# Kernel tuning notes

Hardware: AMD Instinct MI355X
Metric: run time of the kernel (lower is better)

The kernel has to match this reference:

```python
import jax, jax.numpy as jnp
import numpy as np

OBS_DIM = 64; ACT_DIM = 18; INTER = 64; COMMAND = 32
UNITS = ACT_DIM + COMMAND + INTER  # 114; neuron order: [motor, command, inter]
Q_HIDDEN = max(32, UNITS)
B, T = 2048, 64
ODE_UNFOLDS = 6
EPS = 1e-8


def _build_wiring(seed=0):
    """NCP sparse wiring: sensory->inter, inter->command, command recurrent, command->motor."""
    rng = np.random.default_rng(seed)
    adj = np.zeros((UNITS, UNITS), np.float32)   # [pre, post]
    sens = np.zeros((OBS_DIM, UNITS), np.float32)
    motor = np.arange(ACT_DIM)
    cmd = np.arange(ACT_DIM, ACT_DIM + COMMAND)
    inter = np.arange(ACT_DIM + COMMAND, UNITS)
    for s in range(OBS_DIM):
        for d in rng.choice(inter, size=8, replace=False):
            sens[s, d] = rng.choice([-1.0, 1.0])
    for i in inter:
        for d in rng.choice(cmd, size=8, replace=False):
            adj[i, d] = rng.choice([-1.0, 1.0])
    for _ in range(32):
        adj[rng.choice(cmd), rng.choice(cmd)] = rng.choice([-1.0, 1.0])
    for m in motor:
        for s in rng.choice(cmd, size=8, replace=False):
            adj[s, m] = rng.choice([-1.0, 1.0])
    return adj, sens


def setup_inputs() -> dict:
    key = jax.random.key(0)
    ks = jax.random.split(key, 16)
    adj, sens = _build_wiring()
    u = lambda k, shape, lo, hi: jax.random.uniform(k, shape, jnp.float32, lo, hi)
    return {
        "obs": jax.random.normal(ks[0], (B, T, OBS_DIM), jnp.float32),
        "hidden": jnp.zeros((B, UNITS), jnp.float32),
        "input_w": jnp.ones((OBS_DIM,), jnp.float32),
        "input_b": jnp.zeros((OBS_DIM,), jnp.float32),
        "sensory_w": u(ks[1], (OBS_DIM, UNITS), 0.001, 1.0),
        "sensory_mu": u(ks[2], (OBS_DIM, UNITS), 0.3, 0.8),
        "sensory_sigma": u(ks[3], (OBS_DIM, UNITS), 3.0, 8.0),
        "sensory_erev": jnp.asarray(sens),
        "sensory_mask": jnp.asarray(np.abs(sens)),
        "w": u(ks[4], (UNITS, UNITS), 0.001, 1.0),
        "mu": u(ks[5], (UNITS, UNITS), 0.3, 0.8),
        "sigma": u(ks[6], (UNITS, UNITS), 3.0, 8.0),
        "erev": jnp.asarray(adj),
        "mask": jnp.asarray(np.abs(adj)),
        "gleak": u(ks[7], (UNITS,), 0.001, 1.0),
        "vleak": u(ks[8], (UNITS,), -0.2, 0.2),
        "cm": u(ks[9], (UNITS,), 0.4, 0.6),
        "q_w1": jax.random.normal(ks[10], (UNITS, Q_HIDDEN), jnp.float32) / np.sqrt(UNITS).astype(np.float32),
        "q_b1": jnp.zeros((Q_HIDDEN,), jnp.float32),
        "q_w2": jax.random.normal(ks[11], (Q_HIDDEN, ACT_DIM), jnp.float32) / np.sqrt(Q_HIDDEN).astype(np.float32),
        "q_b2": jnp.zeros((ACT_DIM,), jnp.float32),
    }


def _ltc_forward(obs, hidden, input_w, input_b, sensory_w, sensory_mu, sensory_sigma,
                 sensory_erev, sensory_mask, w, mu, sigma, erev, mask, gleak, vleak, cm):
    sw = sensory_w * sensory_mask          # sparse sensory synapses (S, U)
    ww = w * mask                          # sparse recurrent synapses (U, U)
    cm_t = cm * ODE_UNFOLDS                # cm / (elapsed_time / ode_unfolds), elapsed_time = 1.0

    @jax.checkpoint
    def step(h, x):
        xi = x * input_w + input_b                                                    # (B, S) affine input map
        s_act = sw * jax.nn.sigmoid((xi[:, :, None] - sensory_mu) * sensory_sigma)    # (B, S, U)
        w_num_s = jnp.sum(s_act * sensory_erev, axis=1)                               # (B, U)
        w_den_s = jnp.sum(s_act, axis=1)                                              # (B, U)

        def unfold(v, _):
            act = ww * jax.nn.sigmoid((v[:, :, None] - mu) * sigma)                   # (B, U, U)
            num = cm_t * v + gleak * vleak + jnp.sum(act * erev, axis=1) + w_num_s
            den = cm_t + gleak + jnp.sum(act, axis=1) + w_den_s
            return num / (den + EPS), None

        v, _ = jax.lax.scan(unfold, h, None, length=ODE_UNFOLDS)
        return v, None

    h, _ = jax.lax.scan(step, hidden, jnp.swapaxes(obs, 0, 1))  # scan over time
    return h


def reference(obs, hidden, input_w, input_b, sensory_w, sensory_mu, sensory_sigma,
              sensory_erev, sensory_mask, w, mu, sigma, erev, mask, gleak, vleak, cm,
              q_w1, q_b1, q_w2, q_b2):
    h = _ltc_forward(obs, hidden, input_w, input_b, sensory_w, sensory_mu, sensory_sigma,
                     sensory_erev, sensory_mask, w, mu, sigma, erev, mask, gleak, vleak, cm)
    q = jax.nn.relu(h @ q_w1 + q_b1) @ q_w2 + q_b2  # Q-head over full hidden state
    return q, h
```

## Files before the change

### kernel.cpp

```cpp
#include <hip/hip_runtime.h>

#define UNITS   114
#define SDIM    64
#define ACT     18
#define TSTEPS  64

#define CR 13
#define CS 9
#define ER_CAP 704
#define MSTRIDE 24

#define LOG2E 1.4426950408889634f
#define EPS   1e-8f

typedef float v2f __attribute__((ext_vector_type(2)));
__device__ __forceinline__ v2f fma2(v2f a, v2f b, v2f c) {
  return __builtin_elementwise_fma(a, b, c);
}
__device__ __forceinline__ float bperm(int addr, float v) {
  return __int_as_float(__builtin_amdgcn_ds_bpermute(addr, __float_as_int(v)));
}
__device__ __forceinline__ float dperm(int addr, float v) {
  return __int_as_float(__builtin_amdgcn_ds_permute(addr, __float_as_int(v)));
}
__device__ __forceinline__ void wsync() {
  __builtin_amdgcn_fence(__ATOMIC_ACQ_REL, "wavefront");
  __builtin_amdgcn_wave_barrier();
}
__device__ __forceinline__ int canonLane(int u) { return (u >= 64) ? (u - 64) : u; }

__device__ __forceinline__ int kthSetBit(unsigned long long m, int k) {
  int pos = 0;
#pragma unroll
  for (int ww = 32; ww >= 1; ww >>= 1) {
    const unsigned long long lowMask = ((1ull << ww) - 1ull);
    const int c = __popcll(m & lowMask);
    if (k >= c) { k -= c; m >>= ww; pos += ww; }
  }
  return pos;
}

__global__ __launch_bounds__(64) void build_all(
    const float* __restrict__ w,  const float* __restrict__ mu,
    const float* __restrict__ sigma, const float* __restrict__ erev,
    const float* __restrict__ mask,
    const float* __restrict__ sw, const float* __restrict__ smu,
    const float* __restrict__ ssg, const float* __restrict__ serev,
    const float* __restrict__ smask,
    float4* __restrict__ recP4, float2* __restrict__ recP2, int* __restrict__ recAd,
    float4* __restrict__ senP4, float2* __restrict__ senP2, int* __restrict__ senAd,
    int* __restrict__ meta)
{
  const int l = threadIdx.x;
  __shared__ short ePre[ER_CAP], ePIdx[ER_CAP];
  __shared__ int deg[64], off[65];
  __shared__ int pLane[64], pF0[64], pRole[64];
  __shared__ int contIdx[64], contOwn[64], splitRole[64], split2[64], ownP[128];
  __shared__ int rcv[64];

  contIdx[l] = 0; contOwn[l] = 0; splitRole[l] = -1; split2[l] = 0;
  ownP[2*l] = -1; ownP[2*l+1] = -1;
  pLane[l] = 0; pF0[l] = 0; pRole[l] = 0;

  if (blockIdx.x == 0) {
    int d = 0;
    if (l < 50) {
      for (int base = 18; base < 114; base += 16) {
        float mv[16];
#pragma unroll
        for (int q = 0; q < 16; ++q) mv[q] = mask[(base + q)*UNITS + l];
#pragma unroll
        for (int q = 0; q < 16; ++q) d += (mv[q] != 0.f) ? 1 : 0;
      }
    }
    deg[l] = (l < 50) ? d : 0;
    __syncthreads();
    if (l == 0) { int a = 0; for (int j = 0; j < 64; ++j) { off[j] = a; a += deg[j]; } off[64] = a; }
    __syncthreads();
    if (l < 50) {
      int o = off[l];
      for (int base = 18; base < 114; base += 16) {
        float mv[16];
#pragma unroll
        for (int q = 0; q < 16; ++q) mv[q] = mask[(base + q)*UNITS + l];
#pragma unroll
        for (int q = 0; q < 16; ++q)
          if (mv[q] != 0.f) { ePre[o] = (short)(base + q); ePIdx[o] = (short)l; ++o; }
      }
    }
    if (l == 0) {
      int lam = 0, f = 0, pc = 0;
      for (int p = 0; p < 50; ++p) {
        const int dd = deg[p];
        if (pc == 2 || f == CR || dd > 3*CR - f) { ++lam; f = 0; pc = 0; }
        if (lam > 63) lam = 63;
        pLane[p] = lam; pF0[p] = f; pRole[p] = pc;
        ownP[2*lam + pc] = p;
        const int owner = lam, role = pc; ++pc;
        const int take = dd < (CR - f) ? dd : (CR - f);
        f += take; int rem = dd - take;
        if (rem > 0) {
          splitRole[owner] = role; split2[owner] = (rem > CR) ? 1 : 0;
          ++lam; if (lam > 63) lam = 63; contIdx[lam] = 1; contOwn[lam] = owner; pc = 1;
          const int t2 = rem < CR ? rem : CR; f = t2; rem -= t2;
          if (rem > 0) { ++lam; if (lam > 63) lam = 63; contIdx[lam] = 2; contOwn[lam] = owner; pc = 1; f = rem; }
        }
      }
    }
    __syncthreads();
    int dA = (contIdx[l] == 1) ? contOwn[l] : -1;
    int dB = (contIdx[l] == 2) ? contOwn[l] : -1;
    rcv[l] = 0; __syncthreads();
    if (dA >= 0) rcv[dA] = 1;
    __syncthreads();
    { const unsigned long long rM = __ballot(rcv[l] != 0), dM = __ballot(dA < 0);
      if (dA < 0) dA = kthSetBit(~rM, __popcll(dM & ((1ull << l) - 1ull))); }
    __syncthreads();
    rcv[l] = 0; __syncthreads();
    if (dB >= 0) rcv[dB] = 1;
    __syncthreads();
    { const unsigned long long rM = __ballot(rcv[l] != 0), dM = __ballot(dB < 0);
      if (dB < 0) dB = kthSetBit(~rM, __popcll(dM & ((1ull << l) - 1ull))); }
    {
      int* M = meta + l * MSTRIDE;
      M[0] = dA * 4; M[1] = dB * 4;
      const float s1A = (splitRole[l] == 0) ? 1.f : 0.f, s1B = (splitRole[l] == 1) ? 1.f : 0.f;
      M[2] = __float_as_int(s1A); M[3] = __float_as_int(s1B);
      const float s2 = split2[l] ? 1.f : 0.f;
      M[4] = __float_as_int(s1A * s2); M[5] = __float_as_int(s1B * s2);
      const int uA = ownP[2*l], uB = ownP[2*l+1];
      M[6] = ((uA >= 0) ? uA : 128 + l) * 4;
      M[7] = ((uB >= 0) ? uB : 192 + l) * 4;
      M[8] = (uA >= 0) ? uA : 0;
      M[9] = (uB >= 0) ? uB : 0;
    }
    for (int t = l; t < CR*64; t += 64) {
      recP4[t] = make_float4(0.f,0.f,0.f,0.f); recP2[t] = make_float2(0.f,0.f); recAd[t] = 0;
    }
    __syncthreads();
    {
      const int E = off[64];
      for (int e = l; e < E; e += 64) {
        const int pre = ePre[e], pj = ePIdx[e];
        const int r  = e - off[pj];
        const int dd = deg[pj], f0 = pF0[pj], role0 = pRole[pj];
        const int take = dd < (CR - f0) ? dd : (CR - f0);
        int lane = pLane[pj], slot, role;
        if (r < take)            { slot = f0 + r;        role = role0; }
        else if (r < take + CR)  { lane += 1; slot = r - take;      role = 0; }
        else                     { lane += 2; slot = r - take - CR; role = 0; }
        if (lane > 63) lane = 63;
        const int idx = pre * UNITS + pj;
        const float sg = sigma[idx];
        const float nsgl = -sg * LOG2E, msl = mu[idx] * sg * LOG2E;
        const float wd = w[idx], wn = wd * erev[idx];
        const int tt = slot * 64 + lane;
        recP4[tt] = make_float4(nsgl, msl, role ? 0.f : wn, role ? 0.f : wd);
        recP2[tt] = role ? make_float2(wn, wd) : make_float2(0.f, 0.f);
        recAd[tt] = pre * 4;
      }
    }
  } else {
    int d = 0;
    {
      const int col = 50 + l;
      for (int base = 0; base < 64; base += 16) {
        float mv[16];
#pragma unroll
        for (int q = 0; q < 16; ++q) mv[q] = smask[(base + q)*UNITS + col];
#pragma unroll
        for (int q = 0; q < 16; ++q) d += (mv[q] != 0.f) ? 1 : 0;
      }
    }
    deg[l] = d;
    __syncthreads();
    if (l == 0) { int a = 0; for (int j = 0; j < 64; ++j) { off[j] = a; a += deg[j]; } off[64] = a; }
    __syncthreads();
    {
      int o = off[l]; const int col = 50 + l;
      for (int base = 0; base < 64; base += 16) {
        float mv[16];
#pragma unroll
        for (int q = 0; q < 16; ++q) mv[q] = smask[(base + q)*UNITS + col];
#pragma unroll
        for (int q = 0; q < 16; ++q)
          if (mv[q] != 0.f) { ePre[o] = (short)(base + q); ePIdx[o] = (short)l; ++o; }
      }
    }
    if (l == 0) {
      int lam = 0, f = 0, pc = 0;
      for (int p = 0; p < 64; ++p) {
        const int dd = deg[p];
        if (pc == 2 || f == CS || dd > 3*CS - f) { ++lam; f = 0; pc = 0; }
        if (lam > 63) lam = 63;
        pLane[p] = lam; pF0[p] = f; pRole[p] = pc;
        ownP[2*lam + pc] = p;
        const int owner = lam, role = pc; ++pc;
        const int take = dd < (CS - f) ? dd : (CS - f);
        f += take; int rem = dd - take;
        if (rem > 0) {
          splitRole[owner] = role; split2[owner] = (rem > CS) ? 1 : 0;
          ++lam; if (lam > 63) lam = 63; contIdx[lam] = 1; contOwn[lam] = owner; pc = 1;
          const int t2 = rem < CS ? rem : CS; f = t2; rem -= t2;
          if (rem > 0) { ++lam; if (lam > 63) lam = 63; contIdx[lam] = 2; contOwn[lam] = owner; pc = 1; f = rem; }
        }
      }
    }
    __syncthreads();
    int dA = (contIdx[l] == 1) ? contOwn[l] : -1;
    int dB = (contIdx[l] == 2) ? contOwn[l] : -1;
    rcv[l] = 0; __syncthreads();
    if (dA >= 0) rcv[dA] = 1;
    __syncthreads();
    { const unsigned long long rM = __ballot(rcv[l] != 0), dM = __ballot(dA < 0);
      if (dA < 0) dA = kthSetBit(~rM, __popcll(dM & ((1ull << l) - 1ull))); }
    __syncthreads();
    rcv[l] = 0; __syncthreads();
    if (dB >= 0) rcv[dB] = 1;
    __syncthreads();
    { const unsigned long long rM = __ballot(rcv[l] != 0), dM = __ballot(dB < 0);
      if (dB < 0) dB = kthSetBit(~rM, __popcll(dM & ((1ull << l) - 1ull))); }
    __syncthreads();
    int rA = (ownP[2*l]   >= 0) ? canonLane(50 + ownP[2*l])   : -1;
    int rB = (ownP[2*l+1] >= 0) ? canonLane(50 + ownP[2*l+1]) : -1;
    rcv[l] = 0; __syncthreads();
    if (rA >= 0) rcv[rA] = 1;
    __syncthreads();
    const int isRcvA = rcv[l];
    { const unsigned long long rM = __ballot(isRcvA != 0), dM = __ballot(rA < 0);
      if (rA < 0) rA = kthSetBit(~rM, __popcll(dM & ((1ull << l) - 1ull))); }
    __syncthreads();
    rcv[l] = 0; __syncthreads();
    if (rB >= 0) rcv[rB] = 1;
    __syncthreads();
    { const unsigned long long rM = __ballot(rcv[l] != 0), dM = __ballot(rB < 0);
      if (rB < 0) rB = kthSetBit(~rM, __popcll(dM & ((1ull << l) - 1ull))); }
    {
      int* M = meta + l * MSTRIDE;
      M[10] = dA * 4; M[11] = dB * 4;
      const float s1A = (splitRole[l] == 0) ? 1.f : 0.f, s1B = (splitRole[l] == 1) ? 1.f : 0.f;
      M[12] = __float_as_int(s1A); M[13] = __float_as_int(s1B);
      const float s2 = split2[l] ? 1.f : 0.f;
      M[14] = __float_as_int(s1A * s2); M[15] = __float_as_int(s1B * s2);
      M[16] = rA * 4; M[17] = rB * 4;
      M[18] = __float_as_int(isRcvA ? 1.f : 0.f);
      M[19] = __float_as_int(isRcvA ? 0.f : 1.f);
      const int pA = ownP[2*l], pB = ownP[2*l+1];
      M[20] = (pA >= 0) ? 50 + pA : 0;
      M[21] = (pB >= 0) ? 50 + pB : 0;
    }
    for (int t = l; t < CS*64; t += 64) {
      senP4[t] = make_float4(0.f,0.f,0.f,0.f); senP2[t] = make_float2(0.f,0.f); senAd[t] = 0;
    }
    __syncthreads();
    {
      const int E = off[64];
      for (int e = l; e < E; e += 64) {
        const int pre = ePre[e], pj = ePIdx[e];
        const int r  = e - off[pj];
        const int dd = deg[pj], f0 = pF0[pj], role0 = pRole[pj];
        const int take = dd < (CS - f0) ? dd : (CS - f0);
        int lane = pLane[pj], slot, role;
        if (r < take)            { slot = f0 + r;        role = role0; }
        else if (r < take + CS)  { lane += 1; slot = r - take;      role = 0; }
        else                     { lane += 2; slot = r - take - CS; role = 0; }
        if (lane > 63) lane = 63;
        const int col = 50 + pj;
        const int idx = pre * UNITS + col;
        const float sg = ssg[idx];
        const float nsgl = -sg * LOG2E, msl = smu[idx] * sg * LOG2E;
        const float wd = sw[idx], wn = wd * serev[idx];
        const int tt = slot * 64 + lane;
        senP4[tt] = make_float4(nsgl, msl, role ? 0.f : wn, role ? 0.f : wd);
        senP2[tt] = role ? make_float2(wn, wd) : make_float2(0.f, 0.f);
        senAd[tt] = pre * 4;
      }
    }
  }
}

__global__ __launch_bounds__(64, 2) void ltc_run(
    const float* __restrict__ obs,     const float* __restrict__ hidden,
    const float* __restrict__ input_w, const float* __restrict__ input_b,
    const float* __restrict__ gleak,   const float* __restrict__ vleak,
    const float* __restrict__ cm,
    const float* __restrict__ q_w1, const float* __restrict__ q_b1,
    const float* __restrict__ q_w2, const float* __restrict__ q_b2,
    const float4* __restrict__ recP4, const float2* __restrict__ recP2,
    const int* __restrict__ recAd,
    const float4* __restrict__ senP4, const float2* __restrict__ senP2,
    const int* __restrict__ senAd,
    const int* __restrict__ meta, float* __restrict__ out, int B)
{
  const int l = threadIdx.x, b = blockIdx.x;
  __shared__ float mirror[256];
  char* mbase = (char*)mirror;

  float rNS[CR], rMS[CR]; v2f rWA[CR], rWB[CR]; int rad[CR];
#pragma unroll
  for (int s = 0; s < CR; ++s) {
    const float4 p4 = recP4[s*64 + l]; const float2 p2 = recP2[s*64 + l];
    rNS[s] = p4.x; rMS[s] = p4.y; rWA[s] = (v2f){p4.z, p4.w};
    rWB[s] = (v2f){p2.x, p2.y}; rad[s] = recAd[s*64 + l];
  }
  float sNS[CS], sMS[CS]; v2f sWA[CS], sWB[CS]; int sad[CS];
#pragma unroll
  for (int s = 0; s < CS; ++s) {
    const float4 p4 = senP4[s*64 + l]; const float2 p2 = senP2[s*64 + l];
    sNS[s] = p4.x; sMS[s] = p4.y; sWA[s] = (v2f){p4.z, p4.w};
    sWB[s] = (v2f){p2.x, p2.y}; sad[s] = senAd[s*64 + l];
  }

  const int* M = meta + l * MSTRIDE;
  const int   rPush1 = M[0], rPush2 = M[1];
  const v2f gR1A = {__int_as_float(M[2]), __int_as_float(M[2])};
  const v2f gR1B = {__int_as_float(M[3]), __int_as_float(M[3])};
  const v2f gR2A = {__int_as_float(M[4]), __int_as_float(M[4])};
  const v2f gR2B = {__int_as_float(M[5]), __int_as_float(M[5])};
  const int   rWrA = M[6], rWrB = M[7], rUA = M[8], rUB = M[9];
  const int   sPush1 = M[10], sPush2 = M[11];
  const v2f gS1A = {__int_as_float(M[12]), __int_as_float(M[12])};
  const v2f gS1B = {__int_as_float(M[13]), __int_as_float(M[13])};
  const v2f gS2A = {__int_as_float(M[14]), __int_as_float(M[14])};
  const v2f gS2B = {__int_as_float(M[15]), __int_as_float(M[15])};
  const int   sRtA = M[16], sRtB = M[17];
  const float sRndA = __int_as_float(M[18]), sRndB = __int_as_float(M[19]);
  const int   sUA = M[20], sUB = M[21];

  const float cmA  = cm[rUA]*6.f, glvA  = gleak[rUA]*vleak[rUA], cgA  = cm[rUA]*6.f + gleak[rUA] + EPS;
  const float cmB  = cm[rUB]*6.f, glvB  = gleak[rUB]*vleak[rUB], cgB  = cm[rUB]*6.f + gleak[rUB] + EPS;
  const float cmSA = cm[sUA]*6.f, glvSA = gleak[sUA]*vleak[sUA], cgSA = cm[sUA]*6.f + gleak[sUA] + EPS;
  const float cmSB = cm[sUB]*6.f, glvSB = gleak[sUB]*vleak[sUB], cgSB = cm[sUB]*6.f + gleak[sUB] + EPS;

  const int  iUnit = (l < 50) ? 64 + l : l;
  const int  iWr   = iUnit * 4;
  float vIn = hidden[(size_t)b*UNITS + iUnit];
  float vPA = hidden[(size_t)b*UNITS + rUA];
  float vPB = hidden[(size_t)b*UNITS + rUB];

  mirror[l] = hidden[(size_t)b*UNITS + l];
  if (l < 50) mirror[64 + l] = hidden[(size_t)b*UNITS + 64 + l];

  const float iw = input_w[l], ibv = input_b[l];
  const float* ob = obs + (size_t)b*(TSTEPS*SDIM) + l;
  float xr = ob[0];

  for (int t = 0; t < TSTEPS; ++t) {
    const float xi = xr * iw + ibv;
    if (t + 1 < TSTEPS) xr = ob[(t + 1) * SDIM];

    float aI, bI;
    {
      float uu[CS];
#pragma unroll
      for (int s = 0; s < CS; ++s) {
        float z = fmaf(bperm(sad[s], xi), sNS[s], sMS[s]);
        z = fminf(z, 30.f);
        uu[s] = 1.f + __builtin_amdgcn_exp2f(z);
      }
      float sg[CS];
#pragma unroll
      for (int q = 0; q < 4; ++q) {
        const float p = uu[2*q] * uu[2*q+1];
        const float r = __builtin_amdgcn_rcpf(p);
        sg[2*q]   = uu[2*q+1] * r;
        sg[2*q+1] = uu[2*q]   * r;
      }
      sg[8] = __builtin_amdgcn_rcpf(uu[8]);
      v2f a0 = {0.f,0.f}, a1 = {0.f,0.f}, b0 = {0.f,0.f}, b1 = {0.f,0.f};
#pragma unroll
      for (int s = 0; s < CS; ++s) {
        const v2f s2 = {sg[s], sg[s]};
        if (s & 1) { a1 = fma2(sWA[s], s2, a1); b1 = fma2(sWB[s], s2, b1); }
        else       { a0 = fma2(sWA[s], s2, a0); b0 = fma2(sWB[s], s2, b0); }
      }
      v2f cA = a0 + a1, cB = b0 + b1;
      const v2f m1 = {dperm(sPush1, cA.x), dperm(sPush1, cA.y)};
      const v2f m2 = {dperm(sPush2, cA.x), dperm(sPush2, cA.y)};
      v2f tA = fma2(gS1A, m1, cA); tA = fma2(gS2A, m2, tA);
      v2f tB = fma2(gS1B, m1, cB); tB = fma2(gS2B, m2, tB);
      const float rdA = __builtin_amdgcn_rcpf(cgSA + tA.y);
      const float aA = cmSA * rdA, bA = (glvSA + tA.x) * rdA;
      const float rdB = __builtin_amdgcn_rcpf(cgSB + tB.y);
      const float aB = cmSB * rdB, bB = (glvSB + tB.x) * rdB;
      const float ra1 = dperm(sRtA, aA), rb1 = dperm(sRtA, bA);
      const float ra2 = dperm(sRtB, aB), rb2 = dperm(sRtB, bB);
      aI = sRndA*ra1 + sRndB*ra2;
      bI = sRndA*rb1 + sRndB*rb2;
    }

#pragma unroll 1
    for (int u_ = 0; u_ < 6; ++u_) {
      wsync();
      float uu[CR];
#pragma unroll
      for (int s = 0; s < CR; ++s) {
        const float pv = *(const float*)(mbase + rad[s]);
        float z = fmaf(pv, rNS[s], rMS[s]);
        z = fminf(z, 30.f);
        uu[s] = 1.f + __builtin_amdgcn_exp2f(z);
      }
      float sg[CR];
#pragma unroll
      for (int q = 0; q < 6; ++q) {
        const float p = uu[2*q] * uu[2*q+1];
        const float r = __builtin_amdgcn_rcpf(p);
        sg[2*q]   = uu[2*q+1] * r;
        sg[2*q+1] = uu[2*q]   * r;
      }
      sg[12] = __builtin_amdgcn_rcpf(uu[12]);
      v2f a0 = {0.f,0.f}, a1 = {0.f,0.f}, b0 = {0.f,0.f}, b1 = {0.f,0.f};
#pragma unroll
      for (int s = 0; s < CR; ++s) {
        const v2f s2 = {sg[s], sg[s]};
        if (s & 1) { a1 = fma2(rWA[s], s2, a1); b1 = fma2(rWB[s], s2, b1); }
        else       { a0 = fma2(rWA[s], s2, a0); b0 = fma2(rWB[s], s2, b0); }
      }
      v2f aA = a0 + a1, aB = b0 + b1;
      const v2f m1 = {dperm(rPush1, aA.x), dperm(rPush1, aA.y)};
      const v2f m2 = {dperm(rPush2, aA.x), dperm(rPush2, aA.y)};
      v2f tA = fma2(gR1A, m1, aA); tA = fma2(gR2A, m2, tA);
      v2f tB = fma2(gR1B, m1, aB); tB = fma2(gR2B, m2, tB);

      vPA = (fmaf(cmA, vPA, glvA) + tA.x) * __builtin_amdgcn_rcpf(cgA + tA.y);
      vPB = (fmaf(cmB, vPB, glvB) + tB.x) * __builtin_amdgcn_rcpf(cgB + tB.y);
      vIn = fmaf(aI, vIn, bI);
      wsync();
      *(float*)(mbase + rWrA) = vPA;
      *(float*)(mbase + rWrB) = vPB;
      *(float*)(mbase + iWr)  = vIn;
    }
  }
  wsync();

  float* __restrict__ outH = out + (size_t)B * ACT;
  outH[(size_t)b*UNITS + l] = mirror[l];
  if (l < 50) outH[(size_t)b*UNITS + 64 + l] = mirror[64 + l];

  const int j2 = (l < 50) ? 64 + l : l;
  float h1 = q_b1[l], h2 = q_b1[j2];
  for (int i = 0; i < UNITS; ++i) {
    const float hv = mirror[i];
    h1 = fmaf(hv, q_w1[i*UNITS + l],  h1);
    h2 = fmaf(hv, q_w1[i*UNITS + j2], h2);
  }
  h1 = fmaxf(h1, 0.f); h2 = fmaxf(h2, 0.f);
  wsync();
  mirror[l] = h1;
  if (l < 50) mirror[64 + l] = h2;
  wsync();
  if (l < ACT) {
    float q = q_b2[l];
    for (int i = 0; i < UNITS; ++i) q = fmaf(mirror[i], q_w2[i*ACT + l], q);
    out[(size_t)b*ACT + l] = q;
  }
}

extern "C" void kernel_launch(void* const* d_in, const int* in_sizes, int n_in,
                              void* d_out, int out_size, void* d_ws, size_t ws_size,
                              hipStream_t stream)
{
  const float* obs           = (const float*)d_in[0];
  const float* hidden        = (const float*)d_in[1];
  const float* input_w       = (const float*)d_in[2];
  const float* input_b       = (const float*)d_in[3];
  const float* sensory_w     = (const float*)d_in[4];
  const float* sensory_mu    = (const float*)d_in[5];
  const float* sensory_sigma = (const float*)d_in[6];
  const float* sensory_erev  = (const float*)d_in[7];
  const float* sensory_mask  = (const float*)d_in[8];
  const float* w             = (const float*)d_in[9];
  const float* mu            = (const float*)d_in[10];
  const float* sigma         = (const float*)d_in[11];
  const float* erev          = (const float*)d_in[12];
  const float* mask          = (const float*)d_in[13];
  const float* gleak         = (const float*)d_in[14];
  const float* vleak         = (const float*)d_in[15];
  const float* cm            = (const float*)d_in[16];
  const float* q_w1          = (const float*)d_in[17];
  const float* q_b1          = (const float*)d_in[18];
  const float* q_w2          = (const float*)d_in[19];
  const float* q_b2          = (const float*)d_in[20];

  char* ws = (char*)d_ws;
  float4* recP4 = (float4*)(ws);
  float2* recP2 = (float2*)(ws + 13312);
  int*    recAd = (int*)   (ws + 19968);
  float4* senP4 = (float4*)(ws + 23296);
  float2* senP2 = (float2*)(ws + 32512);
  int*    senAd = (int*)   (ws + 37120);
  int*    meta  = (int*)   (ws + 39424);

  build_all<<<2, 64, 0, stream>>>(
      w, mu, sigma, erev, mask,
      sensory_w, sensory_mu, sensory_sigma, sensory_erev, sensory_mask,
      recP4, recP2, recAd, senP4, senP2, senAd, meta);

  const int B = in_sizes[0] / (TSTEPS * SDIM);
  ltc_run<<<B, 64, 0, stream>>>(
      obs, hidden, input_w, input_b, gleak, vleak, cm,
      q_w1, q_b1, q_w2, q_b2,
      recP4, recP2, recAd, senP4, senP2, senAd, meta,
      (float*)d_out, B);
}
```

Baseline: 398.6 us.

## Software-pipeline next timestep's sensory stage into the six ODE unfolds

Computes the sensory synapse contributions for timestep t+1 in pieces interleaved across the six recurrent unfolds of timestep t. The sensory work no longer sits on the serial critical path between timesteps and can fill latency gaps around the syncs and exp/rcp chains. It also merges paired reciprocals (triple products for the last three sigmoids, one rcp shared by both denominators) and prefetches observations two steps ahead. In exchange it raises register pressure and slightly changes rounding through the combined reciprocals.

```diff
diff --git a/kernel.cpp b/kernel.cpp
--- a/kernel.cpp
+++ b/kernel.cpp
@@ -343,93 +343,152 @@
 
   const float iw = input_w[l], ibv = input_b[l];
   const float* ob = obs + (size_t)b*(TSTEPS*SDIM) + l;
-  float xr = ob[0];
-
+
+  float aI, bI;
+  {
+    const float xi = fmaf(ob[0], iw, ibv);
+    float uu[CS];
+#pragma unroll
+    for (int s = 0; s < CS; ++s) {
+      float z = fmaf(bperm(sad[s], xi), sNS[s], sMS[s]);
+      z = fminf(z, 30.f);
+      uu[s] = 1.f + __builtin_amdgcn_exp2f(z);
+    }
+    float sg[CS];
+#pragma unroll
+    for (int q = 0; q < 4; ++q) {
+      const float p = uu[2*q] * uu[2*q+1];
+      const float r = __builtin_amdgcn_rcpf(p);
+      sg[2*q]   = uu[2*q+1] * r;
+      sg[2*q+1] = uu[2*q]   * r;
+    }
+    sg[8] = __builtin_amdgcn_rcpf(uu[8]);
+    v2f cA = {0.f,0.f}, cB = {0.f,0.f};
+#pragma unroll
+    for (int s = 0; s < CS; ++s) {
+      const v2f s2 = {sg[s], sg[s]};
+      cA = fma2(sWA[s], s2, cA);
+      cB = fma2(sWB[s], s2, cB);
+    }
+    const v2f m1 = {dperm(sPush1, cA.x), dperm(sPush1, cA.y)};
+    const v2f m2 = {dperm(sPush2, cA.x), dperm(sPush2, cA.y)};
+    v2f tA = fma2(gS1A, m1, cA); tA = fma2(gS2A, m2, tA);
+    v2f tB = fma2(gS1B, m1, cB); tB = fma2(gS2B, m2, tB);
+    const float rdA = __builtin_amdgcn_rcpf(cgSA + tA.y);
+    const float aA = cmSA * rdA, bA = (glvSA + tA.x) * rdA;
+    const float rdB = __builtin_amdgcn_rcpf(cgSB + tB.y);
+    const float aB = cmSB * rdB, bB = (glvSB + tB.x) * rdB;
+    const float ra1 = dperm(sRtA, aA), rb1 = dperm(sRtA, bA);
+    const float ra2 = dperm(sRtB, aB), rb2 = dperm(sRtB, bB);
+    aI = sRndA*ra1 + sRndB*ra2;
+    bI = sRndA*rb1 + sRndB*rb2;
+  }
+
+  float xiN = fmaf(ob[SDIM], iw, ibv);
+  float xrC = ob[2*SDIM];
+  float su[CS];
+  v2f acA = {0.f,0.f}, acB = {0.f,0.f};
+  v2f tSA = {0.f,0.f}, tSB = {0.f,0.f};
+  float aIn = 0.f, bIn = 0.f;
+
+  auto unfold = [&](auto chunk) {
+    wsync();
+    float uu[CR];
+#pragma unroll
+    for (int s = 0; s < CR; ++s) {
+      const float pv = *(const float*)(mbase + rad[s]);
+      float z = fmaf(pv, rNS[s], rMS[s]);
+      z = fminf(z, 30.f);
+      uu[s] = 1.f + __builtin_amdgcn_exp2f(z);
+    }
+    chunk();
+    float sg[CR];
+#pragma unroll
+    for (int q = 0; q < 5; ++q) {
+      const float p = uu[2*q] * uu[2*q+1];
+      const float r = __builtin_amdgcn_rcpf(p);
+      sg[2*q]   = uu[2*q+1] * r;
+      sg[2*q+1] = uu[2*q]   * r;
+    }
+    {
+      const float p01 = uu[10]*uu[11];
+      const float r = __builtin_amdgcn_rcpf(p01*uu[12]);
+      const float t12 = uu[12]*r;
+      sg[10] = uu[11]*t12; sg[11] = uu[10]*t12; sg[12] = p01*r;
+    }
+    v2f a0 = {0.f,0.f}, a1 = {0.f,0.f}, b0 = {0.f,0.f}, b1 = {0.f,0.f};
+#pragma unroll
+    for (int s = 0; s < CR; ++s) {
+      const v2f s2 = {sg[s], sg[s]};
+      if (s & 1) { a1 = fma2(rWA[s], s2, a1); b1 = fma2(rWB[s], s2, b1); }
+      else       { a0 = fma2(rWA[s], s2, a0); b0 = fma2(rWB[s], s2, b0); }
+    }
+    v2f aA = a0 + a1, aB = b0 + b1;
+    const v2f m1 = {dperm(rPush1, aA.x), dperm(rPush1, aA.y)};
+    const v2f m2 = {dperm(rPush2, aA.x), dperm(rPush2, aA.y)};
+    v2f tA = fma2(gR1A, m1, aA); tA = fma2(gR2A, m2, tA);
+    v2f tB = fma2(gR1B, m1, aB); tB = fma2(gR2B, m2, tB);
+    const float dAq = cgA + tA.y, dBq = cgB + tB.y;
+    const float rr = __builtin_amdgcn_rcpf(dAq * dBq);
+    vPA = (fmaf(cmA, vPA, glvA) + tA.x) * (dBq * rr);
+    vPB = (fmaf(cmB, vPB, glvB) + tB.x) * (dAq * rr);
+    vIn = fmaf(aI, vIn, bI);
+    wsync();
+    *(float*)(mbase + rWrA) = vPA;
+    *(float*)(mbase + rWrB) = vPB;
+    *(float*)(mbase + iWr)  = vIn;
+  };
+
+  auto sExp = [&](int s) {
+    float z = fmaf(bperm(sad[s], xiN), sNS[s], sMS[s]);
+    z = fminf(z, 30.f);
+    su[s] = 1.f + __builtin_amdgcn_exp2f(z);
+  };
+  auto sPair = [&](int s0) {
+    const float p = su[s0] * su[s0+1];
+    const float r = __builtin_amdgcn_rcpf(p);
+    const float g0 = su[s0+1] * r, g1 = su[s0] * r;
+    acA = fma2(sWA[s0],   (v2f){g0,g0}, acA);
+    acA = fma2(sWA[s0+1], (v2f){g1,g1}, acA);
+    acB = fma2(sWB[s0],   (v2f){g0,g0}, acB);
+    acB = fma2(sWB[s0+1], (v2f){g1,g1}, acB);
+  };
+
+#pragma unroll 1
   for (int t = 0; t < TSTEPS; ++t) {
-    const float xi = xr * iw + ibv;
-    if (t + 1 < TSTEPS) xr = ob[(t + 1) * SDIM];
-
-    float aI, bI;
-    {
-      float uu[CS];
-#pragma unroll
-      for (int s = 0; s < CS; ++s) {
-        float z = fmaf(bperm(sad[s], xi), sNS[s], sMS[s]);
-        z = fminf(z, 30.f);
-        uu[s] = 1.f + __builtin_amdgcn_exp2f(z);
-      }
-      float sg[CS];
-#pragma unroll
-      for (int q = 0; q < 4; ++q) {
-        const float p = uu[2*q] * uu[2*q+1];
-        const float r = __builtin_amdgcn_rcpf(p);
-        sg[2*q]   = uu[2*q+1] * r;
-        sg[2*q+1] = uu[2*q]   * r;
-      }
-      sg[8] = __builtin_amdgcn_rcpf(uu[8]);
-      v2f a0 = {0.f,0.f}, a1 = {0.f,0.f}, b0 = {0.f,0.f}, b1 = {0.f,0.f};
-#pragma unroll
-      for (int s = 0; s < CS; ++s) {
-        const v2f s2 = {sg[s], sg[s]};
-        if (s & 1) { a1 = fma2(sWA[s], s2, a1); b1 = fma2(sWB[s], s2, b1); }
-        else       { a0 = fma2(sWA[s], s2, a0); b0 = fma2(sWB[s], s2, b0); }
-      }
-      v2f cA = a0 + a1, cB = b0 + b1;
-      const v2f m1 = {dperm(sPush1, cA.x), dperm(sPush1, cA.y)};
-      const v2f m2 = {dperm(sPush2, cA.x), dperm(sPush2, cA.y)};
-      v2f tA = fma2(gS1A, m1, cA); tA = fma2(gS2A, m2, tA);
-      v2f tB = fma2(gS1B, m1, cB); tB = fma2(gS2B, m2, tB);
-      const float rdA = __builtin_amdgcn_rcpf(cgSA + tA.y);
-      const float aA = cmSA * rdA, bA = (glvSA + tA.x) * rdA;
-      const float rdB = __builtin_amdgcn_rcpf(cgSB + tB.y);
-      const float aB = cmSB * rdB, bB = (glvSB + tB.x) * rdB;
+    unfold([&]{ sExp(0); sExp(1); });
+    unfold([&]{ sExp(2); sExp(3); sPair(0); });
+    unfold([&]{ sExp(4); sExp(5); sPair(2); });
+    unfold([&]{ sExp(6); sExp(7); sExp(8); sPair(4); });
+    unfold([&]{
+      const float p67 = su[6] * su[7];
+      const float r = __builtin_amdgcn_rcpf(p67 * su[8]);
+      const float t67 = su[8] * r;
+      const float g6 = su[7]*t67, g7 = su[6]*t67, g8 = p67*r;
+      acA = fma2(sWA[6], (v2f){g6,g6}, acA); acB = fma2(sWB[6], (v2f){g6,g6}, acB);
+      acA = fma2(sWA[7], (v2f){g7,g7}, acA); acB = fma2(sWB[7], (v2f){g7,g7}, acB);
+      acA = fma2(sWA[8], (v2f){g8,g8}, acA); acB = fma2(sWB[8], (v2f){g8,g8}, acB);
+      const v2f m1 = {dperm(sPush1, acA.x), dperm(sPush1, acA.y)};
+      const v2f m2 = {dperm(sPush2, acA.x), dperm(sPush2, acA.y)};
+      tSA = fma2(gS1A, m1, acA); tSA = fma2(gS2A, m2, tSA);
+      tSB = fma2(gS1B, m1, acB); tSB = fma2(gS2B, m2, tSB);
+    });
+    unfold([&]{
+      const float dA_ = cgSA + tSA.y, dB_ = cgSB + tSB.y;
+      const float rr = __builtin_amdgcn_rcpf(dA_ * dB_);
+      const float rdA = dB_ * rr, rdB = dA_ * rr;
+      const float aA = cmSA * rdA, bA = (glvSA + tSA.x) * rdA;
+      const float aB = cmSB * rdB, bB = (glvSB + tSB.x) * rdB;
       const float ra1 = dperm(sRtA, aA), rb1 = dperm(sRtA, bA);
       const float ra2 = dperm(sRtB, aB), rb2 = dperm(sRtB, bB);
-      aI = sRndA*ra1 + sRndB*ra2;
-      bI = sRndA*rb1 + sRndB*rb2;
-    }
-
-#pragma unroll 1
-    for (int u_ = 0; u_ < 6; ++u_) {
-      wsync();
-      float uu[CR];
-#pragma unroll
-      for (int s = 0; s < CR; ++s) {
-        const float pv = *(const float*)(mbase + rad[s]);
-        float z = fmaf(pv, rNS[s], rMS[s]);
-        z = fminf(z, 30.f);
-        uu[s] = 1.f + __builtin_amdgcn_exp2f(z);
-      }
-      float sg[CR];
-#pragma unroll
-      for (int q = 0; q < 6; ++q) {
-        const float p = uu[2*q] * uu[2*q+1];
-        const float r = __builtin_amdgcn_rcpf(p);
-        sg[2*q]   = uu[2*q+1] * r;
-        sg[2*q+1] = uu[2*q]   * r;
-      }
-      sg[12] = __builtin_amdgcn_rcpf(uu[12]);
-      v2f a0 = {0.f,0.f}, a1 = {0.f,0.f}, b0 = {0.f,0.f}, b1 = {0.f,0.f};
-#pragma unroll
-      for (int s = 0; s < CR; ++s) {
-        const v2f s2 = {sg[s], sg[s]};
-        if (s & 1) { a1 = fma2(rWA[s], s2, a1); b1 = fma2(rWB[s], s2, b1); }
-        else       { a0 = fma2(rWA[s], s2, a0); b0 = fma2(rWB[s], s2, b0); }
-      }
-      v2f aA = a0 + a1, aB = b0 + b1;
-      const v2f m1 = {dperm(rPush1, aA.x), dperm(rPush1, aA.y)};
-      const v2f m2 = {dperm(rPush2, aA.x), dperm(rPush2, aA.y)};
-      v2f tA = fma2(gR1A, m1, aA); tA = fma2(gR2A, m2, tA);
-      v2f tB = fma2(gR1B, m1, aB); tB = fma2(gR2B, m2, tB);
-
-      vPA = (fmaf(cmA, vPA, glvA) + tA.x) * __builtin_amdgcn_rcpf(cgA + tA.y);
-      vPB = (fmaf(cmB, vPB, glvB) + tB.x) * __builtin_amdgcn_rcpf(cgB + tB.y);
-      vIn = fmaf(aI, vIn, bI);
-      wsync();
-      *(float*)(mbase + rWrA) = vPA;
-      *(float*)(mbase + rWrB) = vPB;
-      *(float*)(mbase + iWr)  = vIn;
-    }
+      aIn = sRndA*ra1 + sRndB*ra2;
+      bIn = sRndA*rb1 + sRndB*rb2;
+    });
+    aI = aIn; bI = bIn;
+    xiN = fmaf(xrC, iw, ibv);
+    const int tn = (t + 3 < TSTEPS) ? (t + 3) : (TSTEPS - 1);
+    xrC = ob[tn * SDIM];
+    acA = (v2f){0.f,0.f}; acB = (v2f){0.f,0.f};
   }
   wsync();
 
```

Measured after the change: 382.6 us. 1.04x faster.
